# Performance work log

Hardware: AMD Instinct MI355X
Metric: run time of the kernel (lower is better)

## Reference

```python
import jax, jax.numpy as jnp
import numpy as np

NFFT = 512
HOP = 256
N_FREQ = NFFT // 2


def _imdct_kernels():
    # Matches _get_imdct_kernels: windowed IMDCT cosine basis, shape [nfft, nfft//2]
    def kernel_fn(time, freq):
        win = np.sin(np.pi * (2 * time + 1) / (2.0 * NFFT))
        return np.cos(np.pi / NFFT * (2 * time + 1 + NFFT / 2.0) * (freq + 0.5)) * win
    k = np.fromfunction(kernel_fn, (NFFT, N_FREQ), dtype=np.float64)
    return jnp.asarray(k.astype(np.float32))  # [nfft, n_freq]


def setup_inputs() -> dict:
    key = jax.random.key(0)
    spec = jax.random.normal(key, (16, 1, N_FREQ, 4096), dtype=jnp.float32)
    return {"spec": spec, "kernels": _imdct_kernels()}


def reference(spec, kernels):
    # spec: [B, 1, n_freq, T]; kernels: [nfft, n_freq]
    B, _, _, T = spec.shape
    # conv2d with (n_freq,1) kernel == per-frame basis matmul over frequency
    frames = jnp.einsum('bft,kf->btk', spec[:, 0], kernels) * (4.0 / NFFT)  # [B, T, nfft]
    # conv_transpose2d with identity-diagonal kernel and stride=hop == overlap-add
    L = (T - 1) * HOP + NFFT
    idx = jnp.arange(T)[:, None] * HOP + jnp.arange(NFFT)[None, :]  # [T, nfft]
    out = jnp.zeros((B, L), dtype=spec.dtype).at[:, idx].add(frames)
    return out
```

## Files before the change

### kernel.cpp

```cpp
#include <hip/hip_runtime.h>
#include <hip/hip_bf16.h>
#include <stdint.h>

#define NFREQ 256
#define NB 16
#define NT 4096
#define LOUT 1048832
#define SPAD_FRAMES 4098
#define SPAD_PER_B (SPAD_FRAMES * NFREQ)

typedef __bf16 bf16;
typedef __bf16 bf16x8 __attribute__((ext_vector_type(8)));
typedef float floatx4 __attribute__((ext_vector_type(4)));

__device__ inline bf16 f2bf(float x) {
    union { float f; uint32_t u; } v; v.f = x;
    uint32_t r = (v.u + 0x7fffu + ((v.u >> 16) & 1u)) >> 16;
    union { uint16_t u; bf16 b; } o; o.u = (uint16_t)r;
    return o.b;
}

__global__ __launch_bounds__(256) void transpose_cvt(const float* __restrict__ spec,
                                                     bf16* __restrict__ spad) {
    __shared__ bf16 tile[64][72];
    int b  = blockIdx.z;
    int f0 = blockIdx.y * 64;
    int t0 = blockIdx.x * 64;
    int tid = threadIdx.x;

    int fl = tid >> 2, tq = tid & 3;
    const float* src = spec + ((size_t)b * NFREQ + (f0 + fl)) * NT + t0 + tq * 16;
    for (int i = 0; i < 4; ++i) {
        float4 v = reinterpret_cast<const float4*>(src)[i];
        int tl = tq * 16 + i * 4;
        tile[tl + 0][fl] = f2bf(v.x);
        tile[tl + 1][fl] = f2bf(v.y);
        tile[tl + 2][fl] = f2bf(v.z);
        tile[tl + 3][fl] = f2bf(v.w);
    }
    __syncthreads();
    int tl = tid >> 2, fq = tid & 3;
    bf16* dst = spad + ((size_t)b * SPAD_FRAMES + (1 + t0 + tl)) * NFREQ + f0 + fq * 16;
    const uint4* lsrc = reinterpret_cast<const uint4*>(&tile[tl][fq * 16]);
    reinterpret_cast<uint4*>(dst)[0] = lsrc[0];
    reinterpret_cast<uint4*>(dst)[1] = lsrc[1];
}

__global__ __launch_bounds__(256) void build_kb(const float* __restrict__ ker,
                                                bf16* __restrict__ kb,
                                                bf16* __restrict__ spad) {
    int blk = blockIdx.x;
    int tid = threadIdx.x;
    if (blk < 256) {
        int base = blk * 512 + tid;
        for (int h = 0; h < 2; ++h) {
            int idx = base + h * 256;
            int r = idx >> 9, f = idx & 511;
            float v = (f < 256) ? ker[(r + 256) * 256 + f] : ker[r * 256 + (f - 256)];
            kb[idx] = f2bf(v * 0.0078125f);
        }
    } else {
        int b = blk - 256;
        size_t base = (size_t)b * SPAD_PER_B;
        spad[base + tid] = f2bf(0.0f);
        spad[base + (size_t)4097 * NFREQ + tid] = f2bf(0.0f);
    }
}

__device__ inline void load_lds16(const bf16* g, bf16* l) {
    __builtin_amdgcn_global_load_lds((__attribute__((address_space(1))) void*)g,
                                     (__attribute__((address_space(3))) void*)l,
                                     16, 0, 0);
}

__global__ __launch_bounds__(256) void imdct_gemm(const bf16* __restrict__ spad,
                                                  const bf16* __restrict__ kb,
                                                  float* __restrict__ out) {
    __shared__ bf16 As[128 * 32];
    __shared__ bf16 Bs[128 * 32];

    int jt = blockIdx.x;
    int nt = blockIdx.y;
    int b  = blockIdx.z;
    int tid  = threadIdx.x;
    int lane = tid & 63;
    int w    = tid >> 6;
    int wm = w >> 1, wn = w & 1;
    int j0 = jt * 128;
    int n0 = nt * 128;

    const bf16* Ab = spad + (size_t)b * SPAD_PER_B;

    floatx4 acc[4][4] = {};

    int chunk = lane & 3;
    int rlane = lane >> 2;
    int row = lane & 15, q = lane >> 4;

    for (int kk = 0; kk < 512; kk += 32) {
        for (int c = 0; c < 2; ++c) {
            int m = w * 32 + c * 16 + rlane;
            int j = j0 + m; if (j > 4096) j = 4096;
            const bf16* g = Ab + (size_t)j * 256 + kk + chunk * 8;
            load_lds16(g, As + (w * 32 + c * 16) * 32);
        }
        for (int c = 0; c < 2; ++c) {
            int n = w * 32 + c * 16 + rlane;
            const bf16* g = kb + (size_t)(n0 + n) * 512 + kk + chunk * 8;
            load_lds16(g, Bs + (w * 32 + c * 16) * 32);
        }
        __syncthreads();

        bf16x8 af[4], bf_[4];
        for (int i = 0; i < 4; ++i)
            af[i] = *reinterpret_cast<const bf16x8*>(As + (wm * 64 + i * 16 + row) * 32 + q * 8);
        for (int jn = 0; jn < 4; ++jn)
            bf_[jn] = *reinterpret_cast<const bf16x8*>(Bs + (wn * 64 + jn * 16 + row) * 32 + q * 8);

        for (int i = 0; i < 4; ++i)
            for (int jn = 0; jn < 4; ++jn)
                acc[i][jn] = __builtin_amdgcn_mfma_f32_16x16x32_bf16(af[i], bf_[jn], acc[i][jn], 0, 0, 0);

        __syncthreads();
    }

    for (int i = 0; i < 4; ++i) {
        int jbase = j0 + wm * 64 + i * 16 + q * 4;
        for (int jn = 0; jn < 4; ++jn) {
            int col = n0 + wn * 64 + jn * 16 + row;
            for (int e = 0; e < 4; ++e) {
                int j = jbase + e;
                if (j <= 4096)
                    out[(size_t)b * LOUT + (size_t)j * 256 + col] = acc[i][jn][e];
            }
        }
    }
}

extern "C" void kernel_launch(void* const* d_in, const int* in_sizes, int n_in,
                              void* d_out, int out_size, void* d_ws, size_t ws_size,
                              hipStream_t stream) {
    const float* spec = (const float*)d_in[0];
    const float* ker  = (const float*)d_in[1];
    float* out = (float*)d_out;

    bf16* spad = (bf16*)d_ws;
    bf16* kb   = spad + (size_t)NB * SPAD_PER_B;

    transpose_cvt<<<dim3(NT / 64, NFREQ / 64, NB), 256, 0, stream>>>(spec, spad);
    build_kb<<<272, 256, 0, stream>>>(ker, kb, spad);
    imdct_gemm<<<dim3(33, 2, NB), 256, 0, stream>>>(spad, kb, out);
}
```

Baseline: 156.1 us.

## Fuse spectrum transpose/convert into GEMM and widen N tile to 256

Removes the separate transpose_cvt kernel and padded bf16 staging buffer. The GEMM now reads fp32 spec directly, converts pairs to packed bf16 in registers and writes them transposed into LDS, handling the frame-shift edges with bounds checks. Each block also covers the full 256 output columns with BK=64, uses padded LDS layouts and launch_bounds(256,2). This removes one kernel launch and a round trip of the intermediate through global memory, at the cost of more registers (32 accumulators per thread), half as many blocks, and no async overlap on the A-tile loads.

```diff
diff --git a/kernel.cpp b/kernel.cpp
--- a/kernel.cpp
+++ b/kernel.cpp
@@ -1,137 +1,125 @@
 #include <hip/hip_runtime.h>
-#include <hip/hip_bf16.h>
 #include <stdint.h>
 
 #define NFREQ 256
 #define NB 16
 #define NT 4096
 #define LOUT 1048832
-#define SPAD_FRAMES 4098
-#define SPAD_PER_B (SPAD_FRAMES * NFREQ)
+#define BK 64
+#define AROW_U32 36
+#define BGRP_B 1040
 
 typedef __bf16 bf16;
 typedef __bf16 bf16x8 __attribute__((ext_vector_type(8)));
 typedef float floatx4 __attribute__((ext_vector_type(4)));
 
-__device__ inline bf16 f2bf(float x) {
-    union { float f; uint32_t u; } v; v.f = x;
-    uint32_t r = (v.u + 0x7fffu + ((v.u >> 16) & 1u)) >> 16;
-    union { uint16_t u; bf16 b; } o; o.u = (uint16_t)r;
-    return o.b;
+__device__ inline uint32_t f_as_u(float x) { union { float f; uint32_t u; } v; v.f = x; return v.u; }
+
+__global__ __launch_bounds__(256) void build_kb(const float* __restrict__ ker,
+                                                bf16* __restrict__ kb) {
+    int idx = blockIdx.x * 256 + threadIdx.x;
+    int r = idx >> 9, f = idx & 511;
+    float v = (f < 256) ? ker[(r + 256) * 256 + f] : ker[r * 256 + (f - 256)];
+    uint32_t u = f_as_u(v * 0.0078125f);
+    uint32_t rr = (u + 0x7fffu + ((u >> 16) & 1u)) >> 16;
+    union { uint16_t u; bf16 b; } o; o.u = (uint16_t)rr;
+    kb[idx] = o.b;
 }
 
-__global__ __launch_bounds__(256) void transpose_cvt(const float* __restrict__ spec,
-                                                     bf16* __restrict__ spad) {
-    __shared__ bf16 tile[64][72];
-    int b  = blockIdx.z;
-    int f0 = blockIdx.y * 64;
-    int t0 = blockIdx.x * 64;
-    int tid = threadIdx.x;
-
-    int fl = tid >> 2, tq = tid & 3;
-    const float* src = spec + ((size_t)b * NFREQ + (f0 + fl)) * NT + t0 + tq * 16;
-    for (int i = 0; i < 4; ++i) {
-        float4 v = reinterpret_cast<const float4*>(src)[i];
-        int tl = tq * 16 + i * 4;
-        tile[tl + 0][fl] = f2bf(v.x);
-        tile[tl + 1][fl] = f2bf(v.y);
-        tile[tl + 2][fl] = f2bf(v.z);
-        tile[tl + 3][fl] = f2bf(v.w);
-    }
-    __syncthreads();
-    int tl = tid >> 2, fq = tid & 3;
-    bf16* dst = spad + ((size_t)b * SPAD_FRAMES + (1 + t0 + tl)) * NFREQ + f0 + fq * 16;
-    const uint4* lsrc = reinterpret_cast<const uint4*>(&tile[tl][fq * 16]);
-    reinterpret_cast<uint4*>(dst)[0] = lsrc[0];
-    reinterpret_cast<uint4*>(dst)[1] = lsrc[1];
-}
-
-__global__ __launch_bounds__(256) void build_kb(const float* __restrict__ ker,
-                                                bf16* __restrict__ kb,
-                                                bf16* __restrict__ spad) {
-    int blk = blockIdx.x;
-    int tid = threadIdx.x;
-    if (blk < 256) {
-        int base = blk * 512 + tid;
-        for (int h = 0; h < 2; ++h) {
-            int idx = base + h * 256;
-            int r = idx >> 9, f = idx & 511;
-            float v = (f < 256) ? ker[(r + 256) * 256 + f] : ker[r * 256 + (f - 256)];
-            kb[idx] = f2bf(v * 0.0078125f);
-        }
-    } else {
-        int b = blk - 256;
-        size_t base = (size_t)b * SPAD_PER_B;
-        spad[base + tid] = f2bf(0.0f);
-        spad[base + (size_t)4097 * NFREQ + tid] = f2bf(0.0f);
-    }
-}
-
-__device__ inline void load_lds16(const bf16* g, bf16* l) {
-    __builtin_amdgcn_global_load_lds((__attribute__((address_space(1))) void*)g,
-                                     (__attribute__((address_space(3))) void*)l,
+__device__ inline void load_lds16(const bf16* g, void* l) {
+    __builtin_amdgcn_global_load_lds((const __attribute__((address_space(1))) uint32_t*)g,
+                                     (__attribute__((address_space(3))) uint32_t*)l,
                                      16, 0, 0);
 }
 
-__global__ __launch_bounds__(256) void imdct_gemm(const bf16* __restrict__ spad,
-                                                  const bf16* __restrict__ kb,
-                                                  float* __restrict__ out) {
-    __shared__ bf16 As[128 * 32];
-    __shared__ bf16 Bs[128 * 32];
+__global__ __launch_bounds__(256, 2) void imdct_gemm(const float* __restrict__ spec,
+                                                     const bf16* __restrict__ kb,
+                                                     float* __restrict__ out) {
+    __shared__ uint32_t As[128 * AROW_U32];
+    __shared__ uint8_t  Bs[32 * BGRP_B];
 
-    int jt = blockIdx.x;
-    int nt = blockIdx.y;
-    int b  = blockIdx.z;
-    int tid  = threadIdx.x;
-    int lane = tid & 63;
-    int w    = tid >> 6;
-    int wm = w >> 1, wn = w & 1;
-    int j0 = jt * 128;
-    int n0 = nt * 128;
+    const int jt = blockIdx.x;
+    const int b  = blockIdx.y;
+    const int tid = threadIdx.x;
+    const int lane = tid & 63;
+    const int w = tid >> 6;
+    const int wm = w >> 1, wn = w & 1;
+    const int j0 = jt * 128;
 
-    const bf16* Ab = spad + (size_t)b * SPAD_PER_B;
+    const int q2 = tid & 3;
+    const int p  = (tid >> 2) & 31;
+    const int h  = tid >> 7;
 
-    floatx4 acc[4][4] = {};
+    const int row = lane & 15, q = lane >> 4;
 
-    int chunk = lane & 3;
-    int rlane = lane >> 2;
-    int row = lane & 15, q = lane >> 4;
+    const float* specb = spec + (size_t)b * NFREQ * NT;
 
-    for (int kk = 0; kk < 512; kk += 32) {
-        for (int c = 0; c < 2; ++c) {
-            int m = w * 32 + c * 16 + rlane;
-            int j = j0 + m; if (j > 4096) j = 4096;
-            const bf16* g = Ab + (size_t)j * 256 + kk + chunk * 8;
-            load_lds16(g, As + (w * 32 + c * 16) * 32);
+    floatx4 acc[4][8] = {};
+
+    for (int kki = 0; kki < 8; ++kki) {
+        const int kk = kki * BK;
+        const int fbase = kk & 255;
+        const int tbase = j0 - (kk < 256 ? 1 : 0);
+        const bool edge = (tbase < 0) | (tbase > NT - 128);
+        const float* r0 = specb + (size_t)(fbase + 2 * p) * NT;
+        const float* r1 = r0 + NT;
+
+        for (int i = 0; i < 4; ++i) {
+            const int c = q2 + 16 * h + 4 * i;
+            const int t0 = tbase + c * 4;
+            float v0[4], v1[4];
+            if (!edge) {
+                float4 a4 = *reinterpret_cast<const float4*>(r0 + t0);
+                float4 b4 = *reinterpret_cast<const float4*>(r1 + t0);
+                v0[0] = a4.x; v0[1] = a4.y; v0[2] = a4.z; v0[3] = a4.w;
+                v1[0] = b4.x; v1[1] = b4.y; v1[2] = b4.z; v1[3] = b4.w;
+            } else {
+                for (int e = 0; e < 4; ++e) {
+                    int t = t0 + e;
+                    bool ok = (unsigned)t < (unsigned)NT;
+                    v0[e] = ok ? r0[t] : 0.0f;
+                    v1[e] = ok ? r1[t] : 0.0f;
+                }
+            }
+            for (int e = 0; e < 4; ++e) {
+                uint32_t pk = ((f_as_u(v0[e]) + 0x8000u) >> 16) |
+                              ((f_as_u(v1[e]) + 0x8000u) & 0xffff0000u);
+                As[(c * 4 + e) * AROW_U32 + p] = pk;
+            }
         }
-        for (int c = 0; c < 2; ++c) {
-            int n = w * 32 + c * 16 + rlane;
-            const bf16* g = kb + (size_t)(n0 + n) * 512 + kk + chunk * 8;
-            load_lds16(g, Bs + (w * 32 + c * 16) * 32);
+
+        for (int g = 0; g < 8; ++g) {
+            int grp = w * 8 + g;
+            const bf16* gsrc = kb + (size_t)(grp * 8 + (lane >> 3)) * 512 + kk + (lane & 7) * 8;
+            load_lds16(gsrc, Bs + grp * BGRP_B);
         }
         __syncthreads();
 
-        bf16x8 af[4], bf_[4];
-        for (int i = 0; i < 4; ++i)
-            af[i] = *reinterpret_cast<const bf16x8*>(As + (wm * 64 + i * 16 + row) * 32 + q * 8);
-        for (int jn = 0; jn < 4; ++jn)
-            bf_[jn] = *reinterpret_cast<const bf16x8*>(Bs + (wn * 64 + jn * 16 + row) * 32 + q * 8);
-
-        for (int i = 0; i < 4; ++i)
-            for (int jn = 0; jn < 4; ++jn)
-                acc[i][jn] = __builtin_amdgcn_mfma_f32_16x16x32_bf16(af[i], bf_[jn], acc[i][jn], 0, 0, 0);
-
+        for (int ks = 0; ks < 2; ++ks) {
+            bf16x8 af[4], bfr[8];
+            for (int i = 0; i < 4; ++i)
+                af[i] = *reinterpret_cast<const bf16x8*>(
+                    (const uint8_t*)As + (wm * 64 + i * 16 + row) * 144 + ks * 64 + q * 16);
+            for (int jn = 0; jn < 8; ++jn) {
+                int n = wn * 128 + jn * 16 + row;
+                bfr[jn] = *reinterpret_cast<const bf16x8*>(
+                    Bs + (n >> 3) * BGRP_B + (n & 7) * 128 + ks * 64 + q * 16);
+            }
+            for (int i = 0; i < 4; ++i)
+                for (int jn = 0; jn < 8; ++jn)
+                    acc[i][jn] = __builtin_amdgcn_mfma_f32_16x16x32_bf16(af[i], bfr[jn], acc[i][jn], 0, 0, 0);
+        }
         __syncthreads();
     }
 
     for (int i = 0; i < 4; ++i) {
-        int jbase = j0 + wm * 64 + i * 16 + q * 4;
-        for (int jn = 0; jn < 4; ++jn) {
-            int col = n0 + wn * 64 + jn * 16 + row;
-            for (int e = 0; e < 4; ++e) {
-                int j = jbase + e;
-                if (j <= 4096)
-                    out[(size_t)b * LOUT + (size_t)j * 256 + col] = acc[i][jn][e];
+        int jb = j0 + wm * 64 + i * 16 + q * 4;
+        for (int e = 0; e < 4; ++e) {
+            int j = jb + e;
+            if (j <= 4096) {
+                float* orow = out + (size_t)b * LOUT + (size_t)j * 256;
+                for (int jn = 0; jn < 8; ++jn)
+                    orow[wn * 128 + jn * 16 + row] = acc[i][jn][e];
             }
         }
     }
@@ -144,10 +132,8 @@
     const float* ker  = (const float*)d_in[1];
     float* out = (float*)d_out;
 
-    bf16* spad = (bf16*)d_ws;
-    bf16* kb   = spad + (size_t)NB * SPAD_PER_B;
+    bf16* kb = (bf16*)d_ws;
 
-    transpose_cvt<<<dim3(NT / 64, NFREQ / 64, NB), 256, 0, stream>>>(spec, spad);
-    build_kb<<<272, 256, 0, stream>>>(ker, kb, spad);
-    imdct_gemm<<<dim3(33, 2, NB), 256, 0, stream>>>(spad, kb, out);
+    build_kb<<<512, 256, 0, stream>>>(ker, kb);
+    imdct_gemm<<<dim3(33, NB), 256, 0, stream>>>(spec, kb, out);
 }
```

Measured after the change: 149.3 us. -4.4%, faster.
